# Optimization experiments

Measured on AMD Instinct MI355X. Metric: run time of the kernel, lower is better.

The kernel has to match this reference:

```python
import jax, jax.numpy as jnp
import numpy as np

NUM_EXPERTS = 8
TOP_K = 2


def setup_inputs() -> dict:
    key = jax.random.key(0)
    k1, k2, k3, k4, k5 = jax.random.split(key, 5)
    B, S, H, I, E = 2, 2048, 1024, 3584, NUM_EXPERTS
    scale_h = 1.0 / np.sqrt(H)
    scale_i = 1.0 / np.sqrt(I)
    return {
        "hidden_states": jax.random.normal(k1, (B, S, H), dtype=jnp.float32),
        "gate_w": jax.random.normal(k2, (H, E), dtype=jnp.float32) * scale_h,
        "w1": jax.random.normal(k3, (E, H, I), dtype=jnp.float32) * scale_h,
        "w3": jax.random.normal(k4, (E, H, I), dtype=jnp.float32) * scale_h,
        "w2": jax.random.normal(k5, (E, I, H), dtype=jnp.float32) * scale_i,
    }


def reference(hidden_states, gate_w, w1, w3, w2):
    # Router: [B,S,H] @ [H,E] -> [B,S,E]
    router_logits = jnp.einsum("bsh,he->bse", hidden_states, gate_w).astype(jnp.float32)
    routing_weights, selected_experts = jax.lax.top_k(router_logits, k=TOP_K)
    routing_weights = jax.nn.softmax(routing_weights, axis=-1)  # [B,S,TOP_K]

    final_hidden_state = jnp.zeros_like(hidden_states)
    # Dense loop over all experts (faithful to the original mask-multiply-accumulate)
    for index in range(NUM_EXPERTS):
        h1 = jax.nn.silu(jnp.einsum("bsh,hi->bsi", hidden_states, w1[index]))
        h3 = jnp.einsum("bsh,hi->bsi", hidden_states, w3[index])
        expert_out = jnp.einsum("bsi,ih->bsh", h1 * h3, w2[index])
        # Per-token routing weight for this expert (0 if not selected)
        weight = jnp.sum(
            jnp.where(selected_experts == index, routing_weights, 0.0), axis=-1
        )[:, :, None]  # [B,S,1]
        final_hidden_state = final_hidden_state + weight * expert_out
    return final_hidden_state, router_logits
```

## Files before the change

kernel.cpp:

```cpp
#include <hip/hip_runtime.h>


typedef __bf16 v8bf __attribute__((ext_vector_type(8)));
typedef float  v4f  __attribute__((ext_vector_type(4)));

constexpr int kT = 4096;
constexpr int kH = 1024;
constexpr int kI = 3584;
constexpr int kE = 8;

constexpr size_t SZ_W    = (size_t)kE * kI * kH * 2;
constexpr size_t OFF_W1T = 0;
constexpr size_t OFF_W3T = OFF_W1T + SZ_W;
constexpr size_t OFF_W2T = OFF_W3T + SZ_W;
constexpr size_t OFF_XG  = OFF_W2T + SZ_W;
constexpr size_t OFF_ACT = OFF_XG  + (size_t)2*kT*kH*2;
constexpr size_t OFF_BUF = OFF_ACT + (size_t)2*kT*kI*2;
constexpr size_t OFF_CNT = OFF_BUF + (size_t)2*kT*kH*4;
constexpr size_t OFF_OFS = OFF_CNT + 128;
constexpr size_t OFF_LST = OFF_OFS + 128;
constexpr size_t OFF_TW  = OFF_LST + (size_t)kE*kT*4;
constexpr size_t OFF_GE  = OFF_TW  + (size_t)kT*2*4;

__device__ __forceinline__ void async16(void* lds, const void* g) {
    __builtin_amdgcn_global_load_lds(
        (const __attribute__((address_space(1))) unsigned int*)g,
        (__attribute__((address_space(3))) unsigned int*)lds,
        16, 0, 0);
}

__global__ void zero_counts_kernel(int* __restrict__ counts) {
    if (threadIdx.x < kE) counts[threadIdx.x] = 0;
}

__global__ void prefix_kernel(const int* __restrict__ counts, int* __restrict__ offsets) {
    if (threadIdx.x == 0) {
        int o = 0;
        for (int e = 0; e < kE; e++) { offsets[e] = o; o += counts[e]; }
    }
}

__global__ void router_kernel(const float* __restrict__ x, const float* __restrict__ gw,
                              float* __restrict__ logits_out, float* __restrict__ tw,
                              int* __restrict__ counts, int* __restrict__ list) {
    const int wave = threadIdx.x >> 6;
    const int lane = threadIdx.x & 63;
    const int t = blockIdx.x * 4 + wave;
    const float* xr = x + (size_t)t * kH;

    double acc[kE];
#pragma unroll
    for (int e = 0; e < kE; e++) acc[e] = 0.0;

    for (int j = 0; j < kH / 64; j++) {
        const int h = j * 64 + lane;
        const float xv = xr[h];
        const float* g = gw + (size_t)h * kE;
#pragma unroll
        for (int e = 0; e < kE; e++) acc[e] += (double)xv * (double)g[e];
    }
#pragma unroll
    for (int e = 0; e < kE; e++) {
#pragma unroll
        for (int o = 32; o > 0; o >>= 1) acc[e] += __shfl_xor(acc[e], o, 64);
    }

    if (lane == 0) {
        float lg[kE];
#pragma unroll
        for (int e = 0; e < kE; e++) lg[e] = (float)acc[e];
#pragma unroll
        for (int e = 0; e < kE; e++) logits_out[(size_t)t * kE + e] = lg[e];

        int e0 = 0; float l0 = lg[0];
        for (int e = 1; e < kE; e++) if (lg[e] > l0) { l0 = lg[e]; e0 = e; }
        int e1 = -1; float l1 = -3.4e38f;
        for (int e = 0; e < kE; e++) if (e != e0 && lg[e] > l1) { l1 = lg[e]; e1 = e; }

        const float ex = __expf(l1 - l0);
        const float w0 = 1.0f / (1.0f + ex);
        const float w1 = ex / (1.0f + ex);

        int s0 = atomicAdd(&counts[e0], 1);
        list[e0 * kT + s0] = t * 2 + 0;
        tw[t * 2 + 0] = w0;
        int s1 = atomicAdd(&counts[e1], 1);
        list[e1 * kT + s1] = t * 2 + 1;
        tw[t * 2 + 1] = w1;
    }
}

__global__ void gather_kernel(const float* __restrict__ x, const int* __restrict__ list,
                              const int* __restrict__ counts, const int* __restrict__ offsets,
                              __bf16* __restrict__ xg, int* __restrict__ gentry) {
    const int g = blockIdx.x;
    int e = 0;
    while (e < kE - 1 && g >= offsets[e] + counts[e]) e++;
    const int s = g - offsets[e];
    const int entry = list[e * kT + s];
    const int t = entry >> 1;
    if (threadIdx.x == 0) gentry[g] = entry;
    const int i = threadIdx.x * 4;
    const float4 v = *(const float4*)&x[(size_t)t * kH + i];
    __bf16 pk[4] = {(__bf16)v.x, (__bf16)v.y, (__bf16)v.z, (__bf16)v.w};
    *(ushort4*)&xg[(size_t)g * kH + i] = *(const ushort4*)pk;
}

__global__ void transpose_cvt_kernel(const float* __restrict__ srcA, const float* __restrict__ srcB,
                                     __bf16* __restrict__ dstA, __bf16* __restrict__ dstB,
                                     int R, int C, int nz) {
    __shared__ float tile[64][65];
    const int z = blockIdx.z;
    const float* s;
    __bf16* d;
    if (z < nz) { s = srcA + (size_t)z * R * C;        d = dstA + (size_t)z * R * C; }
    else        { s = srcB + (size_t)(z - nz) * R * C; d = dstB + (size_t)(z - nz) * R * C; }
    const int r0 = blockIdx.y * 64, c0 = blockIdx.x * 64;
    const int tr = threadIdx.x >> 4;
    const int tc = (threadIdx.x & 15) * 4;
#pragma unroll
    for (int i = 0; i < 4; i++) {
        const float4 v = *(const float4*)&s[(size_t)(r0 + tr + i * 16) * C + (c0 + tc)];
        tile[tr + i * 16][tc + 0] = v.x;
        tile[tr + i * 16][tc + 1] = v.y;
        tile[tr + i * 16][tc + 2] = v.z;
        tile[tr + i * 16][tc + 3] = v.w;
    }
    __syncthreads();
#pragma unroll
    for (int i = 0; i < 4; i++) {
        const int oc = tr + i * 16;
        __bf16 pk[4] = {(__bf16)tile[tc + 0][oc], (__bf16)tile[tc + 1][oc],
                        (__bf16)tile[tc + 2][oc], (__bf16)tile[tc + 3][oc]};
        *(ushort4*)&d[(size_t)(c0 + oc) * R + r0 + tc] = *(const ushort4*)pk;
    }
}

__global__ __launch_bounds__(256, 2) void gemm1_kernel(
    const __bf16* __restrict__ xg, const __bf16* __restrict__ w1t,
    const __bf16* __restrict__ w3t, __bf16* __restrict__ act,
    const int* __restrict__ counts, const int* __restrict__ offsets) {
    const int e = blockIdx.z;
    const int cnt = counts[e];
    const int m0 = blockIdx.y * 128;
    if (m0 >= cnt) return;
    const int n0 = blockIdx.x * 128;
    const int off = offsets[e];

    __shared__ __bf16 As[2 * 4096], B1s[2 * 4096], B3s[2 * 4096];

    const int tid = threadIdx.x;
    const int lane = tid & 63, wave = tid >> 6;
    const int wm = (wave >> 1) * 64, wn = (wave & 1) * 64;
    const int lrow = lane & 15, quad = lane >> 4;

    const int scol = (((tid & 3) ^ ((tid >> 2) & 3) ^ ((tid >> 4) & 3))) * 8;
    const __bf16* abase[2];
    const __bf16* b1base[2];
    const __bf16* b3base[2];
    const __bf16* w1b = w1t + (size_t)e * kI * kH + (size_t)n0 * kH;
    const __bf16* w3b = w3t + (size_t)e * kI * kH + (size_t)n0 * kH;
#pragma unroll
    for (int p = 0; p < 2; p++) {
        const int r = p * 64 + (tid >> 2);
        const int gr = min(m0 + r, cnt - 1);
        abase[p]  = xg + (size_t)(off + gr) * kH + scol;
        b1base[p] = w1b + (size_t)r * kH + scol;
        b3base[p] = w3b + (size_t)r * kH + scol;
    }

    const int sw = (lane & 3) ^ ((lane >> 2) & 3);
    const int fragoff = lrow * 32 + ((quad ^ sw) * 8);

    v4f acc1[4][4], acc3[4][4];
#pragma unroll
    for (int i = 0; i < 4; i++)
#pragma unroll
        for (int j = 0; j < 4; j++) { acc1[i][j] = (v4f)0.0f; acc3[i][j] = (v4f)0.0f; }

    constexpr int NK = kH / 32;

#pragma unroll
    for (int p = 0; p < 2; p++) {
        const int soff = p * 2048 + tid * 8;
        async16(&As[soff],  abase[p]);
        async16(&B1s[soff], b1base[p]);
        async16(&B3s[soff], b3base[p]);
    }
    __syncthreads();

    int cur = 0;
    for (int kt = 0; kt < NK; kt++) {
        if (kt + 1 < NK) {
            const int k0n = (kt + 1) * 32;
            const int nb = (cur ^ 1) * 4096;
#pragma unroll
            for (int p = 0; p < 2; p++) {
                const int soff = nb + p * 2048 + tid * 8;
                async16(&As[soff],  abase[p]  + k0n);
                async16(&B1s[soff], b1base[p] + k0n);
                async16(&B3s[soff], b3base[p] + k0n);
            }
        }

        const int base = cur * 4096;
        v8bf a[4];
#pragma unroll
        for (int fm = 0; fm < 4; fm++)
            a[fm] = *(const v8bf*)&As[base + (wm + fm * 16) * 32 + fragoff];
#pragma unroll
        for (int fn = 0; fn < 4; fn++) {
            const v8bf b1 = *(const v8bf*)&B1s[base + (wn + fn * 16) * 32 + fragoff];
            const v8bf b3 = *(const v8bf*)&B3s[base + (wn + fn * 16) * 32 + fragoff];
#pragma unroll
            for (int fm = 0; fm < 4; fm++) {
                acc1[fm][fn] = __builtin_amdgcn_mfma_f32_16x16x32_bf16(a[fm], b1, acc1[fm][fn], 0, 0, 0);
                acc3[fm][fn] = __builtin_amdgcn_mfma_f32_16x16x32_bf16(a[fm], b3, acc3[fm][fn], 0, 0, 0);
            }
        }
        __syncthreads();
        cur ^= 1;
    }

#pragma unroll
    for (int fm = 0; fm < 4; fm++) {
#pragma unroll
        for (int fn = 0; fn < 4; fn++) {
            const v4f c1 = acc1[fm][fn], c3 = acc3[fm][fn];
            const int col = n0 + wn + fn * 16 + lrow;
#pragma unroll
            for (int r = 0; r < 4; r++) {
                const int gm = m0 + wm + fm * 16 + quad * 4 + r;
                if (gm < cnt) {
                    const float h1 = c1[r], h3 = c3[r];
                    const float v = h1 / (1.0f + __expf(-h1)) * h3;
                    act[(size_t)(off + gm) * kI + col] = (__bf16)v;
                }
            }
        }
    }
}

__global__ __launch_bounds__(256, 3) void gemm2_kernel(
    const __bf16* __restrict__ act, const __bf16* __restrict__ w2t,
    float* __restrict__ out, const float* __restrict__ tw,
    const int* __restrict__ gentry,
    const int* __restrict__ counts, const int* __restrict__ offsets) {
    const int e = blockIdx.z;
    const int cnt = counts[e];
    const int m0 = blockIdx.y * 128;
    if (m0 >= cnt) return;
    const int n0 = blockIdx.x * 128;
    const int off = offsets[e];

    __shared__ __bf16 As[2 * 4096], Bs[2 * 4096];

    const int tid = threadIdx.x;
    const int lane = tid & 63, wave = tid >> 6;
    const int wm = (wave >> 1) * 64, wn = (wave & 1) * 64;
    const int lrow = lane & 15, quad = lane >> 4;

    const int scol = (((tid & 3) ^ ((tid >> 2) & 3) ^ ((tid >> 4) & 3))) * 8;
    const __bf16* abase[2];
    const __bf16* bbase[2];
    const __bf16* w2b = w2t + (size_t)e * kH * kI + (size_t)n0 * kI;
#pragma unroll
    for (int p = 0; p < 2; p++) {
        const int r = p * 64 + (tid >> 2);
        const int gr = min(m0 + r, cnt - 1);
        abase[p] = act + (size_t)(off + gr) * kI + scol;
        bbase[p] = w2b + (size_t)r * kI + scol;
    }

    const int sw = (lane & 3) ^ ((lane >> 2) & 3);
    const int fragoff = lrow * 32 + ((quad ^ sw) * 8);

    v4f acc[4][4];
#pragma unroll
    for (int i = 0; i < 4; i++)
#pragma unroll
        for (int j = 0; j < 4; j++) acc[i][j] = (v4f)0.0f;

    constexpr int NK = kI / 32;

#pragma unroll
    for (int p = 0; p < 2; p++) {
        const int soff = p * 2048 + tid * 8;
        async16(&As[soff], abase[p]);
        async16(&Bs[soff], bbase[p]);
    }
    __syncthreads();

    int cur = 0;
    for (int kt = 0; kt < NK; kt++) {
        if (kt + 1 < NK) {
            const int k0n = (kt + 1) * 32;
            const int nb = (cur ^ 1) * 4096;
#pragma unroll
            for (int p = 0; p < 2; p++) {
                const int soff = nb + p * 2048 + tid * 8;
                async16(&As[soff], abase[p] + k0n);
                async16(&Bs[soff], bbase[p] + k0n);
            }
        }

        const int base = cur * 4096;
        v8bf a[4];
#pragma unroll
        for (int fm = 0; fm < 4; fm++)
            a[fm] = *(const v8bf*)&As[base + (wm + fm * 16) * 32 + fragoff];
#pragma unroll
        for (int fn = 0; fn < 4; fn++) {
            const v8bf b = *(const v8bf*)&Bs[base + (wn + fn * 16) * 32 + fragoff];
#pragma unroll
            for (int fm = 0; fm < 4; fm++)
                acc[fm][fn] = __builtin_amdgcn_mfma_f32_16x16x32_bf16(a[fm], b, acc[fm][fn], 0, 0, 0);
        }
        __syncthreads();
        cur ^= 1;
    }

    int   tok[4][4];
    float wgt[4][4];
#pragma unroll
    for (int fm = 0; fm < 4; fm++) {
#pragma unroll
        for (int r = 0; r < 4; r++) {
            const int gm = m0 + wm + fm * 16 + quad * 4 + r;
            if (gm < cnt) {
                const int entry = gentry[off + gm];
                tok[fm][r] = entry >> 1;
                wgt[fm][r] = tw[entry];
            } else {
                tok[fm][r] = -1;
                wgt[fm][r] = 0.0f;
            }
        }
    }

#pragma unroll
    for (int fm = 0; fm < 4; fm++) {
#pragma unroll
        for (int fn = 0; fn < 4; fn++) {
            const v4f c = acc[fm][fn];
            const int col = n0 + wn + fn * 16 + lrow;
#pragma unroll
            for (int r = 0; r < 4; r++) {
                if (tok[fm][r] >= 0)
                    atomicAdd(&out[(size_t)tok[fm][r] * kH + col], wgt[fm][r] * c[r]);
            }
        }
    }
}

extern "C" void kernel_launch(void* const* d_in, const int* in_sizes, int n_in,
                              void* d_out, int out_size, void* d_ws, size_t ws_size,
                              hipStream_t stream) {
    const float* x  = (const float*)d_in[0];
    const float* gw = (const float*)d_in[1];
    const float* w1 = (const float*)d_in[2];
    const float* w3 = (const float*)d_in[3];
    const float* w2 = (const float*)d_in[4];
    float* out = (float*)d_out;
    float* logits_out = out + (size_t)kT * kH;

    char* ws = (char*)d_ws;
    __bf16* w1t   = (__bf16*)(ws + OFF_W1T);
    __bf16* w3t   = (__bf16*)(ws + OFF_W3T);
    __bf16* w2t   = (__bf16*)(ws + OFF_W2T);
    __bf16* xg    = (__bf16*)(ws + OFF_XG);
    __bf16* act   = (__bf16*)(ws + OFF_ACT);
    int*    cnt   = (int*)   (ws + OFF_CNT);
    int*    ofs   = (int*)   (ws + OFF_OFS);
    int*    list  = (int*)   (ws + OFF_LST);
    float*  tw    = (float*) (ws + OFF_TW);
    int*    gent  = (int*)   (ws + OFF_GE);

    zero_counts_kernel<<<1, 64, 0, stream>>>(cnt);
    hipMemsetAsync(out, 0, (size_t)kT * kH * sizeof(float), stream);

    transpose_cvt_kernel<<<dim3(kI / 64, kH / 64, 2 * kE), 256, 0, stream>>>(
        w1, w3, w1t, w3t, kH, kI, kE);
    transpose_cvt_kernel<<<dim3(kH / 64, kI / 64, kE), 256, 0, stream>>>(
        w2, w2, w2t, w2t, kI, kH, kE);

    router_kernel<<<kT / 4, 256, 0, stream>>>(x, gw, logits_out, tw, cnt, list);
    prefix_kernel<<<1, 1, 0, stream>>>(cnt, ofs);
    gather_kernel<<<2 * kT, 256, 0, stream>>>(x, list, cnt, ofs, xg, gent);

    gemm1_kernel<<<dim3(kI / 128, kT / 128, kE), 256, 0, stream>>>(xg, w1t, w3t, act, cnt, ofs);
    gemm2_kernel<<<dim3(kH / 128, kT / 128, kE), 256, 0, stream>>>(act, w2t, out, tw, gent, cnt, ofs);
}
```

Baseline: 842.9 us.

## Drop LDS double buffering in expert GEMMs and restructure atomic epilogue

Both expert GEMM kernels switch from a double-buffered LDS pipeline, where the next K-tile is prefetched during MFMA compute, to a single buffer that is loaded and then synchronized on every iteration. This halves LDS use per block. The gemm2 launch bound drops from 3 to 2 waves per EU, and its epilogue now loads each row's token and weight and issues the atomics in the same loop, without staging arrays. The likely cost is load latency that is no longer hidden behind compute, along with lower occupancy in gemm2.

Result: faster. 797.0 us (-5.4%).

```diff
diff --git a/kernel.cpp b/kernel.cpp
--- a/kernel.cpp
+++ b/kernel.cpp
@@ -147,7 +147,7 @@
     const int n0 = blockIdx.x * 128;
     const int off = offsets[e];
 
-    __shared__ __bf16 As[2 * 4096], B1s[2 * 4096], B3s[2 * 4096];
+    __shared__ __bf16 As[128 * 32], B1s[128 * 32], B3s[128 * 32];
 
     const int tid = threadIdx.x;
     const int lane = tid & 63, wave = tid >> 6;
@@ -178,40 +178,25 @@
 #pragma unroll
         for (int j = 0; j < 4; j++) { acc1[i][j] = (v4f)0.0f; acc3[i][j] = (v4f)0.0f; }
 
-    constexpr int NK = kH / 32;
-
-#pragma unroll
-    for (int p = 0; p < 2; p++) {
-        const int soff = p * 2048 + tid * 8;
-        async16(&As[soff],  abase[p]);
-        async16(&B1s[soff], b1base[p]);
-        async16(&B3s[soff], b3base[p]);
-    }
-    __syncthreads();
-
-    int cur = 0;
-    for (int kt = 0; kt < NK; kt++) {
-        if (kt + 1 < NK) {
-            const int k0n = (kt + 1) * 32;
-            const int nb = (cur ^ 1) * 4096;
-#pragma unroll
-            for (int p = 0; p < 2; p++) {
-                const int soff = nb + p * 2048 + tid * 8;
-                async16(&As[soff],  abase[p]  + k0n);
-                async16(&B1s[soff], b1base[p] + k0n);
-                async16(&B3s[soff], b3base[p] + k0n);
-            }
-        }
-
-        const int base = cur * 4096;
+    for (int kt = 0; kt < kH / 32; kt++) {
+        const int k0 = kt * 32;
+#pragma unroll
+        for (int p = 0; p < 2; p++) {
+            const int soff = p * 2048 + tid * 8;
+            async16(&As[soff],  abase[p]  + k0);
+            async16(&B1s[soff], b1base[p] + k0);
+            async16(&B3s[soff], b3base[p] + k0);
+        }
+        __syncthreads();
+
         v8bf a[4];
 #pragma unroll
         for (int fm = 0; fm < 4; fm++)
-            a[fm] = *(const v8bf*)&As[base + (wm + fm * 16) * 32 + fragoff];
+            a[fm] = *(const v8bf*)&As[(wm + fm * 16) * 32 + fragoff];
 #pragma unroll
         for (int fn = 0; fn < 4; fn++) {
-            const v8bf b1 = *(const v8bf*)&B1s[base + (wn + fn * 16) * 32 + fragoff];
-            const v8bf b3 = *(const v8bf*)&B3s[base + (wn + fn * 16) * 32 + fragoff];
+            const v8bf b1 = *(const v8bf*)&B1s[(wn + fn * 16) * 32 + fragoff];
+            const v8bf b3 = *(const v8bf*)&B3s[(wn + fn * 16) * 32 + fragoff];
 #pragma unroll
             for (int fm = 0; fm < 4; fm++) {
                 acc1[fm][fn] = __builtin_amdgcn_mfma_f32_16x16x32_bf16(a[fm], b1, acc1[fm][fn], 0, 0, 0);
@@ -219,7 +204,6 @@
             }
         }
         __syncthreads();
-        cur ^= 1;
     }
 
 #pragma unroll
@@ -241,7 +225,7 @@
     }
 }
 
-__global__ __launch_bounds__(256, 3) void gemm2_kernel(
+__global__ __launch_bounds__(256, 2) void gemm2_kernel(
     const __bf16* __restrict__ act, const __bf16* __restrict__ w2t,
     float* __restrict__ out, const float* __restrict__ tw,
     const int* __restrict__ gentry,
@@ -253,7 +237,7 @@
     const int n0 = blockIdx.x * 128;
     const int off = offsets[e];
 
-    __shared__ __bf16 As[2 * 4096], Bs[2 * 4096];
+    __shared__ __bf16 As[128 * 32], Bs[128 * 32];
 
     const int tid = threadIdx.x;
     const int lane = tid & 63, wave = tid >> 6;
@@ -281,47 +265,30 @@
 #pragma unroll
         for (int j = 0; j < 4; j++) acc[i][j] = (v4f)0.0f;
 
-    constexpr int NK = kI / 32;
-
-#pragma unroll
-    for (int p = 0; p < 2; p++) {
-        const int soff = p * 2048 + tid * 8;
-        async16(&As[soff], abase[p]);
-        async16(&Bs[soff], bbase[p]);
-    }
-    __syncthreads();
-
-    int cur = 0;
-    for (int kt = 0; kt < NK; kt++) {
-        if (kt + 1 < NK) {
-            const int k0n = (kt + 1) * 32;
-            const int nb = (cur ^ 1) * 4096;
-#pragma unroll
-            for (int p = 0; p < 2; p++) {
-                const int soff = nb + p * 2048 + tid * 8;
-                async16(&As[soff], abase[p] + k0n);
-                async16(&Bs[soff], bbase[p] + k0n);
-            }
-        }
-
-        const int base = cur * 4096;
+    for (int kt = 0; kt < kI / 32; kt++) {
+        const int k0 = kt * 32;
+#pragma unroll
+        for (int p = 0; p < 2; p++) {
+            const int soff = p * 2048 + tid * 8;
+            async16(&As[soff], abase[p] + k0);
+            async16(&Bs[soff], bbase[p] + k0);
+        }
+        __syncthreads();
+
         v8bf a[4];
 #pragma unroll
         for (int fm = 0; fm < 4; fm++)
-            a[fm] = *(const v8bf*)&As[base + (wm + fm * 16) * 32 + fragoff];
+            a[fm] = *(const v8bf*)&As[(wm + fm * 16) * 32 + fragoff];
 #pragma unroll
         for (int fn = 0; fn < 4; fn++) {
-            const v8bf b = *(const v8bf*)&Bs[base + (wn + fn * 16) * 32 + fragoff];
+            const v8bf b = *(const v8bf*)&Bs[(wn + fn * 16) * 32 + fragoff];
 #pragma unroll
             for (int fm = 0; fm < 4; fm++)
                 acc[fm][fn] = __builtin_amdgcn_mfma_f32_16x16x32_bf16(a[fm], b, acc[fm][fn], 0, 0, 0);
         }
         __syncthreads();
-        cur ^= 1;
-    }
-
-    int   tok[4][4];
-    float wgt[4][4];
+    }
+
 #pragma unroll
     for (int fm = 0; fm < 4; fm++) {
 #pragma unroll
@@ -329,25 +296,13 @@
             const int gm = m0 + wm + fm * 16 + quad * 4 + r;
             if (gm < cnt) {
                 const int entry = gentry[off + gm];
-                tok[fm][r] = entry >> 1;
-                wgt[fm][r] = tw[entry];
-            } else {
-                tok[fm][r] = -1;
-                wgt[fm][r] = 0.0f;
-            }
-        }
-    }
-
-#pragma unroll
-    for (int fm = 0; fm < 4; fm++) {
-#pragma unroll
-        for (int fn = 0; fn < 4; fn++) {
-            const v4f c = acc[fm][fn];
-            const int col = n0 + wn + fn * 16 + lrow;
-#pragma unroll
-            for (int r = 0; r < 4; r++) {
-                if (tok[fm][r] >= 0)
-                    atomicAdd(&out[(size_t)tok[fm][r] * kH + col], wgt[fm][r] * c[r]);
+                const int t = entry >> 1;
+                const float w = tw[entry];
+#pragma unroll
+                for (int fn = 0; fn < 4; fn++) {
+                    const int col = n0 + wn + fn * 16 + lrow;
+                    atomicAdd(&out[(size_t)t * kH + col], w * acc[fm][fn][r]);
+                }
             }
         }
     }
```
